# Optimization experiments

Measured on AMD Instinct MI355X. Metric: run time of the kernel, lower is better.

## Reference

```python
import jax, jax.numpy as jnp
import numpy as np

B, S, D = 2, 2048, 2048
H, KVH, HD = 32, 8, 64
GROUPS = H // KVH  # 4
NEG = -1e9


def setup_inputs() -> dict:
    key = jax.random.key(0)
    ks = jax.random.split(key, 5)
    x = jax.random.normal(ks[0], (B, S, D), dtype=jnp.float32)
    # causal additive mask [1,1,S,S]
    causal = jnp.triu(jnp.full((S, S), NEG, dtype=jnp.float32), k=1)[None, None]
    Wq = jax.random.normal(ks[1], (D, D), dtype=jnp.float32) * (D ** -0.5)
    Wk = jax.random.normal(ks[2], (KVH * HD, D), dtype=jnp.float32) * (D ** -0.5)
    Wv = jax.random.normal(ks[3], (KVH * HD, D), dtype=jnp.float32) * (D ** -0.5)
    Wo = jax.random.normal(ks[4], (D, D), dtype=jnp.float32) * (D ** -0.5)
    return {"x": x, "attention_mask": causal, "Wq": Wq, "Wk": Wk, "Wv": Wv, "Wo": Wo}


def reference(x, attention_mask, Wq, Wk, Wv, Wo):
    b, s, _ = x.shape
    # projections (nn.Linear: y = x @ W.T)
    q = (x @ Wq.T).reshape(b, s, H, HD).transpose(0, 2, 1, 3)      # [b,H,s,hd]
    k = (x @ Wk.T).reshape(b, s, KVH, HD).transpose(0, 2, 1, 3)    # [b,KVH,s,hd]
    v = (x @ Wv.T).reshape(b, s, KVH, HD).transpose(0, 2, 1, 3)
    new_kv_cache = (k, v)
    # repeat_interleave over head dim for GQA
    k = jnp.repeat(k, GROUPS, axis=1)  # [b,H,s,hd]
    v = jnp.repeat(v, GROUPS, axis=1)
    scale = 1.0 / jnp.sqrt(jnp.float32(HD))
    scores = jnp.einsum('bhqd,bhkd->bhqk', q, k) * scale
    scores = scores + attention_mask
    attn = jax.nn.softmax(scores.astype(jnp.float32), axis=-1).astype(q.dtype)
    out = jnp.einsum('bhqk,bhkd->bhqd', attn, v)  # [b,H,s,hd]
    out = out.transpose(0, 2, 1, 3).reshape(b, s, H * HD)
    output = out @ Wo.T
    return (output, new_kv_cache[0], new_kv_cache[1])
```

## Files before the change

kernel.cpp:

```cpp
#include <hip/hip_runtime.h>
#include <hip/hip_bf16.h>
#include <stdint.h>

#define B_ 2
#define S_ 2048
#define D_ 2048
#define H_ 32
#define KVH_ 8
#define HD_ 64

typedef __bf16 bf16x8 __attribute__((ext_vector_type(8)));
typedef float f32x4 __attribute__((ext_vector_type(4)));

#define MFMA16(a, b, c) __builtin_amdgcn_mfma_f32_16x16x32_bf16((a), (b), (c), 0, 0, 0)

typedef __attribute__((address_space(1))) void gvoid_t;
typedef __attribute__((address_space(3))) void lvoid_t;

__device__ __forceinline__ void async_ld16(__hip_bfloat16* lds, const __hip_bfloat16* g) {
  __builtin_amdgcn_global_load_lds((gvoid_t*)(void*)(g), (lvoid_t*)(lds), 16, 0, 0);
}

__device__ __forceinline__ unsigned short f2bu(float f) {
  __hip_bfloat16 h = __float2bfloat16(f);
  return *reinterpret_cast<unsigned short*>(&h);
}

__global__ void cast_bf16_kernel(const float* __restrict__ in,
                                 unsigned short* __restrict__ out, int n4) {
  int i = blockIdx.x * blockDim.x + threadIdx.x;
  if (i >= n4) return;
  float4 v = reinterpret_cast<const float4*>(in)[i];
  ushort4 o;
  o.x = f2bu(v.x); o.y = f2bu(v.y); o.z = f2bu(v.z); o.w = f2bu(v.w);
  reinterpret_cast<ushort4*>(out)[i] = o;
}

template <int MODE>
__global__ __launch_bounds__(256, 2)
void gemm_bt(const __hip_bfloat16* __restrict__ A,
             const __hip_bfloat16* __restrict__ W,
             float* __restrict__ Cf, __hip_bfloat16* __restrict__ Cb,
             float* __restrict__ Cf2, __hip_bfloat16* __restrict__ Cb2,
             __hip_bfloat16* __restrict__ Cb3,
             int M, int N, int K) {
  __shared__ __align__(16) __hip_bfloat16 sA[128 * 32];
  __shared__ __align__(16) __hip_bfloat16 sB[128 * 32];
  const int tid = threadIdx.x;
  const int lane = tid & 63;
  const int wv = tid >> 6;
  const int l15 = lane & 15, l4 = lane >> 4;
  const int bm = blockIdx.x * 128, bn = blockIdx.y * 128;
  const int wm = (wv >> 1) * 64, wn = (wv & 1) * 64;

  const int ci0 = tid, ci1 = tid + 256;
  const __hip_bfloat16* gA0 = A + (size_t)(bm + (ci0 >> 2)) * K + (ci0 & 3) * 8;
  const __hip_bfloat16* gA1 = A + (size_t)(bm + (ci1 >> 2)) * K + (ci1 & 3) * 8;
  const __hip_bfloat16* gB0 = W + (size_t)(bn + (ci0 >> 2)) * K + (ci0 & 3) * 8;
  const __hip_bfloat16* gB1 = W + (size_t)(bn + (ci1 >> 2)) * K + (ci1 & 3) * 8;
  __hip_bfloat16* lA0 = &sA[ci0 * 8];
  __hip_bfloat16* lA1 = &sA[ci1 * 8];
  __hip_bfloat16* lB0 = &sB[ci0 * 8];
  __hip_bfloat16* lB1 = &sB[ci1 * 8];

  f32x4 acc[4][4];
#pragma unroll
  for (int i = 0; i < 4; ++i) {
#pragma unroll
    for (int j = 0; j < 4; ++j) acc[i][j] = f32x4{0.f, 0.f, 0.f, 0.f};
  }

  for (int k0 = 0; k0 < K; k0 += 32) {
    async_ld16(lA0, gA0 + k0);
    async_ld16(lA1, gA1 + k0);
    async_ld16(lB0, gB0 + k0);
    async_ld16(lB1, gB1 + k0);
    __syncthreads();
    bf16x8 af[4], bfr[4];
#pragma unroll
    for (int i = 0; i < 4; ++i)
      af[i] = *reinterpret_cast<const bf16x8*>(&sA[(wm + i * 16 + l15) * 32 + l4 * 8]);
#pragma unroll
    for (int j = 0; j < 4; ++j)
      bfr[j] = *reinterpret_cast<const bf16x8*>(&sB[(wn + j * 16 + l15) * 32 + l4 * 8]);
#pragma unroll
    for (int i = 0; i < 4; ++i) {
#pragma unroll
      for (int j = 0; j < 4; ++j) acc[i][j] = MFMA16(af[i], bfr[j], acc[i][j]);
    }
    __syncthreads();
  }

#pragma unroll
  for (int i = 0; i < 4; ++i) {
#pragma unroll
    for (int j = 0; j < 4; ++j) {
      const int col = bn + wn + j * 16 + l15;
#pragma unroll
      for (int r = 0; r < 4; ++r) {
        const int row = bm + wm + i * 16 + l4 * 4 + r;
        const float v = acc[i][j][r];
        if (MODE == 1) {
          Cf[(size_t)row * N + col] = v;
        } else {
          if (bn < 2048) {
            Cb[(size_t)row * 2048 + col] = __float2bfloat16(v);
          } else {
            const int bb = row >> 11, s = row & 2047;
            const int kv = col - 2048;
            if (kv < 512) {
              const int g = kv >> 6, hd = kv & 63;
              const size_t idx = ((size_t)(bb * KVH_ + g) * S_ + s) * HD_ + hd;
              Cf[idx] = v;
              Cb2[idx] = __float2bfloat16(v);
            } else {
              const int vv = kv - 512;
              const int g = vv >> 6, hd = vv & 63;
              const size_t idx = ((size_t)(bb * KVH_ + g) * S_ + s) * HD_ + hd;
              Cf2[idx] = v;
              Cb3[((size_t)(bb * KVH_ + g) * HD_ + hd) * S_ + s] = __float2bfloat16(v);
            }
          }
        }
      }
    }
  }
}

__global__ __launch_bounds__(256, 2)
void attn_fused(const __hip_bfloat16* __restrict__ Qb,
                const __hip_bfloat16* __restrict__ Kb,
                const __hip_bfloat16* __restrict__ Vtb,
                __hip_bfloat16* __restrict__ AOb) {
  __shared__ __align__(16) __hip_bfloat16 sK[2][64 * 64];
  __shared__ __align__(16) __hip_bfloat16 sV[2][64 * 64];
  __shared__ __align__(16) __hip_bfloat16 sP[4 * 2 * 32 * 64];

  const int tid = threadIdx.x;
  const int lane = tid & 63;
  const int wv = tid >> 6;
  const int l15 = lane & 15, l4 = lane >> 4;
  const int qa = blockIdx.x;
  const int qb = 15 - qa;
  const int h = blockIdx.y;
  const int b = blockIdx.z;
  const int g = h >> 2;

  bf16x8 qfA[2][2], qfB[2][2];
  {
    const __hip_bfloat16* QpA =
        Qb + ((size_t)(b * S_ + qa * 128 + wv * 32)) * D_ + h * HD_;
    const __hip_bfloat16* QpB =
        Qb + ((size_t)(b * S_ + qb * 128 + wv * 32)) * D_ + h * HD_;
#pragma unroll
    for (int i = 0; i < 2; ++i) {
#pragma unroll
      for (int c = 0; c < 2; ++c) {
        qfA[i][c] = *reinterpret_cast<const bf16x8*>(
            QpA + (size_t)(i * 16 + l15) * D_ + c * 32 + l4 * 8);
        qfB[i][c] = *reinterpret_cast<const bf16x8*>(
            QpB + (size_t)(i * 16 + l15) * D_ + c * 32 + l4 * 8);
      }
    }
  }

  f32x4 oaccA[2][4], oaccB[2][4];
  f32x4 laccA[2], laccB[2];
#pragma unroll
  for (int i = 0; i < 2; ++i) {
    laccA[i] = f32x4{0.f, 0.f, 0.f, 0.f};
    laccB[i] = f32x4{0.f, 0.f, 0.f, 0.f};
#pragma unroll
    for (int j = 0; j < 4; ++j) {
      oaccA[i][j] = f32x4{0.f, 0.f, 0.f, 0.f};
      oaccB[i][j] = f32x4{0.f, 0.f, 0.f, 0.f};
    }
  }

  bf16x8 vone;
#pragma unroll
  for (int j = 0; j < 8; ++j) vone[j] = (__bf16)1.0f;

  const __hip_bfloat16* Kp = Kb + (size_t)(b * KVH_ + g) * S_ * HD_;
  const __hip_bfloat16* Vp = Vtb + (size_t)(b * KVH_ + g) * HD_ * S_;
  __hip_bfloat16* sPwB = sP + (wv * 2 + 0) * (32 * 64);
  __hip_bfloat16* sPwA = sP + (wv * 2 + 1) * (32 * 64);
  const float CE = 0.125f * 1.4426950408889634f;
  const float MSUB = 8.0f;

  const int p0 = tid, p1 = tid + 256;
  const int r0 = p0 >> 3, c0 = (p0 & 7) ^ (r0 & 7);
  const int r1 = p1 >> 3, c1 = (p1 & 7) ^ (r1 & 7);
  const __hip_bfloat16* gk0 = Kp + (size_t)r0 * HD_ + c0 * 8;
  const __hip_bfloat16* gk1 = Kp + (size_t)r1 * HD_ + c1 * 8;
  const __hip_bfloat16* gv0 = Vp + (size_t)r0 * S_ + c0 * 8;
  const __hip_bfloat16* gv1 = Vp + (size_t)r1 * S_ + c1 * 8;

  auto stage = [&](int buf) {
    async_ld16(&sK[buf][p0 * 8], gk0);
    async_ld16(&sK[buf][p1 * 8], gk1);
    async_ld16(&sV[buf][p0 * 8], gv0);
    async_ld16(&sV[buf][p1 * 8], gv1);
    gk0 += 64 * HD_; gk1 += 64 * HD_;
    gv0 += 64;       gv1 += 64;
  };

  auto pack = [&](f32x4 (&sc)[2][4], int koff, __hip_bfloat16* dst) {
    if (koff >= 0) {
#pragma unroll
      for (int i = 0; i < 2; ++i) {
#pragma unroll
        for (int jn = 0; jn < 4; ++jn) {
          const int kp = koff + jn * 16 + l15;
#pragma unroll
          for (int r = 0; r < 4; ++r) {
            const int qp = wv * 32 + i * 16 + l4 * 4 + r;
            if (kp > qp) sc[i][jn][r] = -3.0e38f;
          }
        }
      }
    }
#pragma unroll
    for (int i = 0; i < 2; ++i) {
#pragma unroll
      for (int jj = 0; jj < 4; ++jj) {
#pragma unroll
        for (int r = 0; r < 4; ++r) {
          const float p = exp2f(fmaf(sc[i][jj][r], CE, -MSUB));
          dst[(i * 16 + l4 * 4 + r) * 64 + ((jj ^ l4) * 16 + l15)] =
              __float2bfloat16(p);
        }
      }
    }
  };

  const int nsteps = 2 * qb + 2;
  const int kiA_max = 2 * qa + 1;
  stage(0);
  for (int ki = 0; ki < nsteps; ++ki) {
    const int cur = ki & 1;
    __syncthreads();
    if (ki + 1 < nsteps) stage(cur ^ 1);
    const bool doA = (ki <= kiA_max);
    const int koB = ((ki >> 1) == qb) ? (ki & 1) * 64 : -1;
    const int koA = ((ki >> 1) == qa) ? (ki & 1) * 64 : -1;

    f32x4 scB[2][4], scA[2][4];
#pragma unroll
    for (int jn = 0; jn < 4; ++jn) {
      const int row = jn * 16 + l15;
      const bf16x8 k0 = *reinterpret_cast<const bf16x8*>(
          &sK[cur][(row * 8 + (l4 ^ (row & 7))) * 8]);
      const bf16x8 k1 = *reinterpret_cast<const bf16x8*>(
          &sK[cur][(row * 8 + ((4 + l4) ^ (row & 7))) * 8]);
#pragma unroll
      for (int i = 0; i < 2; ++i) {
        f32x4 t = f32x4{0.f, 0.f, 0.f, 0.f};
        t = MFMA16(qfB[i][0], k0, t);
        t = MFMA16(qfB[i][1], k1, t);
        scB[i][jn] = t;
      }
      if (doA) {
#pragma unroll
        for (int i = 0; i < 2; ++i) {
          f32x4 t = f32x4{0.f, 0.f, 0.f, 0.f};
          t = MFMA16(qfA[i][0], k0, t);
          t = MFMA16(qfA[i][1], k1, t);
          scA[i][jn] = t;
        }
      }
    }

    pack(scB, koB, sPwB);
    if (doA) pack(scA, koA, sPwA);

    const int gr = (l15 >> 2) & 3;
#pragma unroll
    for (int kc = 0; kc < 2; ++kc) {
      bf16x8 vf[4];
#pragma unroll
      for (int jn = 0; jn < 4; ++jn) {
        const int row = jn * 16 + l15;
        vf[jn] = *reinterpret_cast<const bf16x8*>(
            &sV[cur][(row * 8 + ((kc * 4 + l4) ^ (row & 7))) * 8]);
      }
      const int pcol = (((kc * 2 + (l4 >> 1)) ^ gr) * 16 + (l4 & 1) * 8);
#pragma unroll
      for (int i = 0; i < 2; ++i) {
        const bf16x8 pf = *reinterpret_cast<const bf16x8*>(
            &sPwB[(i * 16 + l15) * 64 + pcol]);
#pragma unroll
        for (int jn = 0; jn < 4; ++jn) oaccB[i][jn] = MFMA16(pf, vf[jn], oaccB[i][jn]);
        laccB[i] = MFMA16(pf, vone, laccB[i]);
      }
      if (doA) {
#pragma unroll
        for (int i = 0; i < 2; ++i) {
          const bf16x8 pf = *reinterpret_cast<const bf16x8*>(
              &sPwA[(i * 16 + l15) * 64 + pcol]);
#pragma unroll
          for (int jn = 0; jn < 4; ++jn) oaccA[i][jn] = MFMA16(pf, vf[jn], oaccA[i][jn]);
          laccA[i] = MFMA16(pf, vone, laccA[i]);
        }
      }
    }
  }

#pragma unroll
  for (int tsel = 0; tsel < 2; ++tsel) {
    const int qt = tsel ? qb : qa;
    f32x4 (&oacc)[2][4] = tsel ? oaccB : oaccA;
    f32x4 (&lacc)[2] = tsel ? laccB : laccA;
#pragma unroll
    for (int i = 0; i < 2; ++i) {
      float inv[4];
#pragma unroll
      for (int r = 0; r < 4; ++r) inv[r] = 1.0f / lacc[i][r];
#pragma unroll
      for (int jn = 0; jn < 4; ++jn) {
#pragma unroll
        for (int r = 0; r < 4; ++r) {
          const int qp = qt * 128 + wv * 32 + i * 16 + l4 * 4 + r;
          AOb[(size_t)(b * S_ + qp) * D_ + h * HD_ + jn * 16 + l15] =
              __float2bfloat16(oacc[i][jn][r] * inv[r]);
        }
      }
    }
  }
}

extern "C" void kernel_launch(void* const* d_in, const int* in_sizes, int n_in,
                              void* d_out, int out_size, void* d_ws, size_t ws_size,
                              hipStream_t stream) {
  (void)in_sizes; (void)n_in; (void)out_size; (void)ws_size;
  const float* x = (const float*)d_in[0];
  const float* Wq = (const float*)d_in[2];
  const float* Wk = (const float*)d_in[3];
  const float* Wv = (const float*)d_in[4];
  const float* Wo = (const float*)d_in[5];

  float* outO = (float*)d_out;
  float* outK = outO + (size_t)B_ * S_ * D_;
  float* outV = outK + (size_t)B_ * KVH_ * S_ * HD_;

  char* p = (char*)d_ws;
  __hip_bfloat16* xb    = (__hip_bfloat16*)p; p += (size_t)B_ * S_ * D_ * 2;
  __hip_bfloat16* Wqkvb = (__hip_bfloat16*)p; p += (size_t)3072 * D_ * 2;
  __hip_bfloat16* Wob   = (__hip_bfloat16*)p; p += (size_t)D_ * D_ * 2;
  __hip_bfloat16* Qbf   = (__hip_bfloat16*)p; p += (size_t)B_ * S_ * D_ * 2;
  __hip_bfloat16* Kbf   = (__hip_bfloat16*)p; p += (size_t)B_ * KVH_ * S_ * HD_ * 2;
  __hip_bfloat16* Vtb   = (__hip_bfloat16*)p; p += (size_t)B_ * KVH_ * S_ * HD_ * 2;
  __hip_bfloat16* AOb   = (__hip_bfloat16*)p; p += (size_t)B_ * S_ * D_ * 2;

  auto cast = [&](const float* src, __hip_bfloat16* dst, size_t n) {
    const int n4 = (int)(n / 4);
    cast_bf16_kernel<<<dim3((n4 + 255) / 256), dim3(256), 0, stream>>>(
        src, (unsigned short*)dst, n4);
  };
  cast(x, xb, (size_t)B_ * S_ * D_);
  cast(Wq, Wqkvb, (size_t)D_ * D_);
  cast(Wk, Wqkvb + (size_t)2048 * D_, (size_t)KVH_ * HD_ * D_);
  cast(Wv, Wqkvb + (size_t)2560 * D_, (size_t)KVH_ * HD_ * D_);
  cast(Wo, Wob, (size_t)D_ * D_);

  gemm_bt<4><<<dim3(32, 24), dim3(256), 0, stream>>>(
      xb, Wqkvb, outK, Qbf, outV, Kbf, Vtb, 4096, 3072, 2048);
  attn_fused<<<dim3(8, 32, 2), dim3(256), 0, stream>>>(Qbf, Kbf, Vtb, AOb);
  gemm_bt<1><<<dim3(32, 16), dim3(256), 0, stream>>>(
      AOb, Wob, outO, nullptr, nullptr, nullptr, nullptr, 4096, 2048, 2048);
}
```

Measured before the change: 333.6 us.

## Split paired query tiles across separate waves with 512-thread attention blocks

```diff
diff --git a/kernel.cpp b/kernel.cpp
--- a/kernel.cpp
+++ b/kernel.cpp
@@ -127,14 +127,14 @@
   }
 }
 
-__global__ __launch_bounds__(256, 2)
+__global__ __launch_bounds__(512, 4)
 void attn_fused(const __hip_bfloat16* __restrict__ Qb,
                 const __hip_bfloat16* __restrict__ Kb,
                 const __hip_bfloat16* __restrict__ Vtb,
                 __hip_bfloat16* __restrict__ AOb) {
   __shared__ __align__(16) __hip_bfloat16 sK[2][64 * 64];
   __shared__ __align__(16) __hip_bfloat16 sV[2][64 * 64];
-  __shared__ __align__(16) __hip_bfloat16 sP[4 * 2 * 32 * 64];
+  __shared__ __align__(16) __hip_bfloat16 sP[8 * 32 * 64];
 
   const int tid = threadIdx.x;
   const int lane = tid & 63;
@@ -142,39 +142,34 @@
   const int l15 = lane & 15, l4 = lane >> 4;
   const int qa = blockIdx.x;
   const int qb = 15 - qa;
+  const int isB = wv >> 2;
+  const int wq = wv & 3;
+  const int qt = isB ? qb : qa;
   const int h = blockIdx.y;
   const int b = blockIdx.z;
   const int g = h >> 2;
 
-  bf16x8 qfA[2][2], qfB[2][2];
+  bf16x8 qf[2][2];
   {
-    const __hip_bfloat16* QpA =
-        Qb + ((size_t)(b * S_ + qa * 128 + wv * 32)) * D_ + h * HD_;
-    const __hip_bfloat16* QpB =
-        Qb + ((size_t)(b * S_ + qb * 128 + wv * 32)) * D_ + h * HD_;
+    const __hip_bfloat16* Qp =
+        Qb + ((size_t)(b * S_ + qt * 128 + wq * 32)) * D_ + h * HD_;
 #pragma unroll
     for (int i = 0; i < 2; ++i) {
 #pragma unroll
       for (int c = 0; c < 2; ++c) {
-        qfA[i][c] = *reinterpret_cast<const bf16x8*>(
-            QpA + (size_t)(i * 16 + l15) * D_ + c * 32 + l4 * 8);
-        qfB[i][c] = *reinterpret_cast<const bf16x8*>(
-            QpB + (size_t)(i * 16 + l15) * D_ + c * 32 + l4 * 8);
-      }
-    }
-  }
-
-  f32x4 oaccA[2][4], oaccB[2][4];
-  f32x4 laccA[2], laccB[2];
+        qf[i][c] = *reinterpret_cast<const bf16x8*>(
+            Qp + (size_t)(i * 16 + l15) * D_ + c * 32 + l4 * 8);
+      }
+    }
+  }
+
+  f32x4 oacc[2][4];
+  f32x4 lacc[2];
 #pragma unroll
   for (int i = 0; i < 2; ++i) {
-    laccA[i] = f32x4{0.f, 0.f, 0.f, 0.f};
-    laccB[i] = f32x4{0.f, 0.f, 0.f, 0.f};
-#pragma unroll
-    for (int j = 0; j < 4; ++j) {
-      oaccA[i][j] = f32x4{0.f, 0.f, 0.f, 0.f};
-      oaccB[i][j] = f32x4{0.f, 0.f, 0.f, 0.f};
-    }
+    lacc[i] = f32x4{0.f, 0.f, 0.f, 0.f};
+#pragma unroll
+    for (int j = 0; j < 4; ++j) oacc[i][j] = f32x4{0.f, 0.f, 0.f, 0.f};
   }
 
   bf16x8 vone;
@@ -183,29 +178,22 @@
 
   const __hip_bfloat16* Kp = Kb + (size_t)(b * KVH_ + g) * S_ * HD_;
   const __hip_bfloat16* Vp = Vtb + (size_t)(b * KVH_ + g) * HD_ * S_;
-  __hip_bfloat16* sPwB = sP + (wv * 2 + 0) * (32 * 64);
-  __hip_bfloat16* sPwA = sP + (wv * 2 + 1) * (32 * 64);
+  __hip_bfloat16* sPw = sP + wv * (32 * 64);
   const float CE = 0.125f * 1.4426950408889634f;
   const float MSUB = 8.0f;
 
-  const int p0 = tid, p1 = tid + 256;
-  const int r0 = p0 >> 3, c0 = (p0 & 7) ^ (r0 & 7);
-  const int r1 = p1 >> 3, c1 = (p1 & 7) ^ (r1 & 7);
-  const __hip_bfloat16* gk0 = Kp + (size_t)r0 * HD_ + c0 * 8;
-  const __hip_bfloat16* gk1 = Kp + (size_t)r1 * HD_ + c1 * 8;
-  const __hip_bfloat16* gv0 = Vp + (size_t)r0 * S_ + c0 * 8;
-  const __hip_bfloat16* gv1 = Vp + (size_t)r1 * S_ + c1 * 8;
+  const int r0 = tid >> 3, c0 = (tid & 7) ^ (r0 & 7);
+  const __hip_bfloat16* gk = Kp + (size_t)r0 * HD_ + c0 * 8;
+  const __hip_bfloat16* gv = Vp + (size_t)r0 * S_ + c0 * 8;
 
   auto stage = [&](int buf) {
-    async_ld16(&sK[buf][p0 * 8], gk0);
-    async_ld16(&sK[buf][p1 * 8], gk1);
-    async_ld16(&sV[buf][p0 * 8], gv0);
-    async_ld16(&sV[buf][p1 * 8], gv1);
-    gk0 += 64 * HD_; gk1 += 64 * HD_;
-    gv0 += 64;       gv1 += 64;
+    async_ld16(&sK[buf][tid * 8], gk);
+    async_ld16(&sV[buf][tid * 8], gv);
+    gk += 64 * HD_;
+    gv += 64;
   };
 
-  auto pack = [&](f32x4 (&sc)[2][4], int koff, __hip_bfloat16* dst) {
+  auto pack = [&](f32x4 (&sc)[2][4], int koff) {
     if (koff >= 0) {
 #pragma unroll
       for (int i = 0; i < 2; ++i) {
@@ -214,7 +202,7 @@
           const int kp = koff + jn * 16 + l15;
 #pragma unroll
           for (int r = 0; r < 4; ++r) {
-            const int qp = wv * 32 + i * 16 + l4 * 4 + r;
+            const int qp = wq * 32 + i * 16 + l4 * 4 + r;
             if (kp > qp) sc[i][jn][r] = -3.0e38f;
           }
         }
@@ -227,7 +215,7 @@
 #pragma unroll
         for (int r = 0; r < 4; ++r) {
           const float p = exp2f(fmaf(sc[i][jj][r], CE, -MSUB));
-          dst[(i * 16 + l4 * 4 + r) * 64 + ((jj ^ l4) * 16 + l15)] =
+          sPw[(i * 16 + l4 * 4 + r) * 64 + ((jj ^ l4) * 16 + l15)] =
               __float2bfloat16(p);
         }
       }
@@ -235,95 +223,69 @@
   };
 
   const int nsteps = 2 * qb + 2;
-  const int kiA_max = 2 * qa + 1;
+  const int kmax = isB ? nsteps : (2 * qa + 2);
   stage(0);
   for (int ki = 0; ki < nsteps; ++ki) {
     const int cur = ki & 1;
     __syncthreads();
     if (ki + 1 < nsteps) stage(cur ^ 1);
-    const bool doA = (ki <= kiA_max);
-    const int koB = ((ki >> 1) == qb) ? (ki & 1) * 64 : -1;
-    const int koA = ((ki >> 1) == qa) ? (ki & 1) * 64 : -1;
-
-    f32x4 scB[2][4], scA[2][4];
-#pragma unroll
-    for (int jn = 0; jn < 4; ++jn) {
-      const int row = jn * 16 + l15;
-      const bf16x8 k0 = *reinterpret_cast<const bf16x8*>(
-          &sK[cur][(row * 8 + (l4 ^ (row & 7))) * 8]);
-      const bf16x8 k1 = *reinterpret_cast<const bf16x8*>(
-          &sK[cur][(row * 8 + ((4 + l4) ^ (row & 7))) * 8]);
-#pragma unroll
-      for (int i = 0; i < 2; ++i) {
-        f32x4 t = f32x4{0.f, 0.f, 0.f, 0.f};
-        t = MFMA16(qfB[i][0], k0, t);
-        t = MFMA16(qfB[i][1], k1, t);
-        scB[i][jn] = t;
-      }
-      if (doA) {
+    if (ki < kmax) {
+      const int ko = ((ki >> 1) == qt) ? (ki & 1) * 64 : -1;
+
+      f32x4 sc[2][4];
+#pragma unroll
+      for (int jn = 0; jn < 4; ++jn) {
+        const int row = jn * 16 + l15;
+        const bf16x8 k0 = *reinterpret_cast<const bf16x8*>(
+            &sK[cur][(row * 8 + (l4 ^ (row & 7))) * 8]);
+        const bf16x8 k1 = *reinterpret_cast<const bf16x8*>(
+            &sK[cur][(row * 8 + ((4 + l4) ^ (row & 7))) * 8]);
 #pragma unroll
         for (int i = 0; i < 2; ++i) {
           f32x4 t = f32x4{0.f, 0.f, 0.f, 0.f};
-          t = MFMA16(qfA[i][0], k0, t);
-          t = MFMA16(qfA[i][1], k1, t);
-          scA[i][jn] = t;
-        }
-      }
-    }
-
-    pack(scB, koB, sPwB);
-    if (doA) pack(scA, koA, sPwA);
-
-    const int gr = (l15 >> 2) & 3;
-#pragma unroll
-    for (int kc = 0; kc < 2; ++kc) {
-      bf16x8 vf[4];
-#pragma unroll
-      for (int jn = 0; jn < 4; ++jn) {
-        const int row = jn * 16 + l15;
-        vf[jn] = *reinterpret_cast<const bf16x8*>(
-            &sV[cur][(row * 8 + ((kc * 4 + l4) ^ (row & 7))) * 8]);
-      }
-      const int pcol = (((kc * 2 + (l4 >> 1)) ^ gr) * 16 + (l4 & 1) * 8);
-#pragma unroll
-      for (int i = 0; i < 2; ++i) {
-        const bf16x8 pf = *reinterpret_cast<const bf16x8*>(
-            &sPwB[(i * 16 + l15) * 64 + pcol]);
-#pragma unroll
-        for (int jn = 0; jn < 4; ++jn) oaccB[i][jn] = MFMA16(pf, vf[jn], oaccB[i][jn]);
-        laccB[i] = MFMA16(pf, vone, laccB[i]);
-      }
-      if (doA) {
+          t = MFMA16(qf[i][0], k0, t);
+          t = MFMA16(qf[i][1], k1, t);
+          sc[i][jn] = t;
+        }
+      }
+
+      pack(sc, ko);
+
+      const int gr = (l15 >> 2) & 3;
+#pragma unroll
+      for (int kc = 0; kc < 2; ++kc) {
+        bf16x8 vf[4];
+#pragma unroll
+        for (int jn = 0; jn < 4; ++jn) {
+          const int row = jn * 16 + l15;
+          vf[jn] = *reinterpret_cast<const bf16x8*>(
+              &sV[cur][(row * 8 + ((kc * 4 + l4) ^ (row & 7))) * 8]);
+        }
+        const int pcol = (((kc * 2 + (l4 >> 1)) ^ gr) * 16 + (l4 & 1) * 8);
 #pragma unroll
         for (int i = 0; i < 2; ++i) {
           const bf16x8 pf = *reinterpret_cast<const bf16x8*>(
-              &sPwA[(i * 16 + l15) * 64 + pcol]);
-#pragma unroll
-          for (int jn = 0; jn < 4; ++jn) oaccA[i][jn] = MFMA16(pf, vf[jn], oaccA[i][jn]);
-          laccA[i] = MFMA16(pf, vone, laccA[i]);
-        }
-      }
-    }
-  }
-
-#pragma unroll
-  for (int tsel = 0; tsel < 2; ++tsel) {
-    const int qt = tsel ? qb : qa;
-    f32x4 (&oacc)[2][4] = tsel ? oaccB : oaccA;
-    f32x4 (&lacc)[2] = tsel ? laccB : laccA;
-#pragma unroll
-    for (int i = 0; i < 2; ++i) {
-      float inv[4];
-#pragma unroll
-      for (int r = 0; r < 4; ++r) inv[r] = 1.0f / lacc[i][r];
-#pragma unroll
-      for (int jn = 0; jn < 4; ++jn) {
-#pragma unroll
-        for (int r = 0; r < 4; ++r) {
-          const int qp = qt * 128 + wv * 32 + i * 16 + l4 * 4 + r;
-          AOb[(size_t)(b * S_ + qp) * D_ + h * HD_ + jn * 16 + l15] =
-              __float2bfloat16(oacc[i][jn][r] * inv[r]);
-        }
+              &sPw[(i * 16 + l15) * 64 + pcol]);
+#pragma unroll
+          for (int jn = 0; jn < 4; ++jn) oacc[i][jn] = MFMA16(pf, vf[jn], oacc[i][jn]);
+          lacc[i] = MFMA16(pf, vone, lacc[i]);
+        }
+      }
+    }
+  }
+
+#pragma unroll
+  for (int i = 0; i < 2; ++i) {
+    float inv[4];
+#pragma unroll
+    for (int r = 0; r < 4; ++r) inv[r] = 1.0f / lacc[i][r];
+#pragma unroll
+    for (int jn = 0; jn < 4; ++jn) {
+#pragma unroll
+      for (int r = 0; r < 4; ++r) {
+        const int qp = qt * 128 + wq * 32 + i * 16 + l4 * 4 + r;
+        AOb[(size_t)(b * S_ + qp) * D_ + h * HD_ + jn * 16 + l15] =
+            __float2bfloat16(oacc[i][jn][r] * inv[r]);
       }
     }
   }
@@ -365,7 +327,7 @@
 
   gemm_bt<4><<<dim3(32, 24), dim3(256), 0, stream>>>(
       xb, Wqkvb, outK, Qbf, outV, Kbf, Vtb, 4096, 3072, 2048);
-  attn_fused<<<dim3(8, 32, 2), dim3(256), 0, stream>>>(Qbf, Kbf, Vtb, AOb);
+  attn_fused<<<dim3(8, 32, 2), dim3(512), 0, stream>>>(Qbf, Kbf, Vtb, AOb);
   gemm_bt<1><<<dim3(32, 16), dim3(256), 0, stream>>>(
       AOb, Wob, outO, nullptr, nullptr, nullptr, nullptr, 4096, 2048, 2048);
 }
```

Result: no change. 327.5 us (-1.8%).
